# Optimization experiments

Measured on AMD Instinct MI355X. Metric: run time of the kernel, lower is better.

## Reference

```python
import jax, jax.numpy as jnp
import numpy as np

LN_EPS = 1e-5


def setup_inputs() -> dict:
    key = jax.random.key(0)
    ks = jax.random.split(key, 8)
    B, C, H, W = 16, 768, 64, 64
    cond_dim = 1024
    inp = {}
    inp["spatial_features"] = jax.random.normal(ks[0], (B, C, H, W), dtype=jnp.float32)
    inp["conditioning"] = jax.random.normal(ks[1], (B, cond_dim), dtype=jnp.float32)
    # conditioning_proj: Linear(cond_dim -> C)
    inp["w_cond"] = jax.random.normal(ks[2], (C, cond_dim), dtype=jnp.float32) * 0.02
    inp["b_cond"] = jnp.zeros((C,), dtype=jnp.float32)
    # MultiheadAttention packed in-projection [3C, C] and bias [3C]
    inp["in_proj_w"] = jax.random.normal(ks[3], (3 * C, C), dtype=jnp.float32) * 0.02
    inp["in_proj_b"] = jnp.zeros((3 * C,), dtype=jnp.float32)
    # MHA out_proj
    inp["attn_out_w"] = jax.random.normal(ks[4], (C, C), dtype=jnp.float32) * 0.02
    inp["attn_out_b"] = jnp.zeros((C,), dtype=jnp.float32)
    # output_proj Linear (dropout is identity at inference)
    inp["w_out"] = jax.random.normal(ks[5], (C, C), dtype=jnp.float32) * 0.02
    inp["b_out"] = jnp.zeros((C,), dtype=jnp.float32)
    # LayerNorm affine
    inp["ln_gamma"] = jnp.ones((C,), dtype=jnp.float32)
    inp["ln_beta"] = jnp.zeros((C,), dtype=jnp.float32)
    return inp


def reference(spatial_features, conditioning, w_cond, b_cond, in_proj_w, in_proj_b,
              attn_out_w, attn_out_b, w_out, b_out, ln_gamma, ln_beta):
    B, C, H, W = spatial_features.shape
    S = H * W
    # [B, C, H, W] -> [B, S, C]
    spatial_flat = spatial_features.reshape(B, C, S).transpose(0, 2, 1)
    # conditioning projection -> single KV token per batch: [B, C]
    cond = conditioning @ w_cond.T + b_cond
    # With a single key, softmax over the key axis is identically 1, so the
    # attention output is exactly the value vector broadcast over all queries;
    # Q and K projections have zero effect on output (and zero gradient).
    wv = in_proj_w[2 * C:]          # value rows of packed in-projection
    bv = in_proj_b[2 * C:]
    v = cond @ wv.T + bv            # [B, C]
    attn = v @ attn_out_w.T + attn_out_b  # MHA out_proj, [B, C]
    # output_proj (dropout = identity in eval)
    proj = attn @ w_out.T + b_out   # [B, C]
    # residual + LayerNorm over channel dim
    x = spatial_flat + proj[:, None, :]  # [B, S, C]
    mu = jnp.mean(x, axis=-1, keepdims=True)
    var = jnp.mean(jnp.square(x - mu), axis=-1, keepdims=True)
    y = (x - mu) * jax.lax.rsqrt(var + LN_EPS) * ln_gamma + ln_beta
    # [B, S, C] -> [B, C, H, W]
    return y.transpose(0, 2, 1).reshape(B, C, H, W)
```

## Files before the change

kernel.cpp:

```cpp
#include <hip/hip_runtime.h>

#define CDIM 768
#define SDIM 4096
#define SV (SDIM / 4)

typedef float nfloat4 __attribute__((ext_vector_type(4)));

__global__ __launch_bounds__(256) void small_gemm_kernel(
    const float* __restrict__ X, const float* __restrict__ W,
    const float* __restrict__ bias, float* __restrict__ out,
    int Cn, int K)
{
    int gid  = blockIdx.x * blockDim.x + threadIdx.x;
    int wid  = gid >> 6;
    int lane = threadIdx.x & 63;
    int total = 16 * Cn;
    if (wid >= total) return;
    int b = wid / Cn;
    int c = wid - b * Cn;
    const float* x = X + (size_t)b * K;
    const float* w = W + (size_t)c * K;
    float acc = 0.f;
    for (int k = lane * 4; k < K; k += 256) {
        float4 xv = *(const float4*)(x + k);
        float4 wv = *(const float4*)(w + k);
        acc += xv.x * wv.x + xv.y * wv.y + xv.z * wv.z + xv.w * wv.w;
    }
#pragma unroll
    for (int m = 32; m; m >>= 1) acc += __shfl_xor(acc, m, 64);
    if (lane == 0) out[wid] = acc + bias[c];
}

__global__ __launch_bounds__(512) void fused_add_ln_1pass(
    const float* __restrict__ sp, const float* __restrict__ proj,
    const float* __restrict__ gamma, const float* __restrict__ beta,
    float* __restrict__ out)
{
    __shared__ float s_proj[CDIM], s_gamma[CDIM], s_beta[CDIM];
    __shared__ float4 red_s[64][8];
    __shared__ float4 red_q[64][8];
    __shared__ float4 red2_s[8][8];
    __shared__ float4 red2_q[8][8];
    __shared__ float4 s_mu[8];
    __shared__ float4 s_rs[8];

    const int b  = blockIdx.y;
    const int s0 = blockIdx.x * 32;
    const int t  = threadIdx.x;
    for (int i = t; i < CDIM; i += 512) {
        s_proj[i]  = proj[b * CDIM + i];
        s_gamma[i] = gamma[i];
        s_beta[i]  = beta[i];
    }
    __syncthreads();

    const int si = t & 7;
    const int cg = t >> 3;
    const int c0 = cg * (CDIM / 64);

    const float4* spv  = (const float4*)(sp  + (size_t)b * CDIM * SDIM + s0) + (size_t)c0 * SV + si;
    nfloat4*      outv = (nfloat4*)     (out + (size_t)b * CDIM * SDIM + s0) + (size_t)c0 * SV + si;

    float4 x[12];
    float sx = 0, sy = 0, sz = 0, sw = 0;
    float qx = 0, qy = 0, qz = 0, qw = 0;
#pragma unroll
    for (int j = 0; j < 12; ++j) {
        float4 v = spv[(size_t)j * SV];
        float  p = s_proj[c0 + j];
        v.x += p; v.y += p; v.z += p; v.w += p;
        x[j] = v;
        sx += v.x; sy += v.y; sz += v.z; sw += v.w;
        qx += v.x * v.x; qy += v.y * v.y; qz += v.z * v.z; qw += v.w * v.w;
    }
    red_s[cg][si] = make_float4(sx, sy, sz, sw);
    red_q[cg][si] = make_float4(qx, qy, qz, qw);
    __syncthreads();

    if (t < 64) {
        const int si2 = t & 7;
        const int h   = t >> 3;
        float4 S = make_float4(0, 0, 0, 0), Q = make_float4(0, 0, 0, 0);
#pragma unroll
        for (int g = h * 8; g < h * 8 + 8; ++g) {
            float4 a = red_s[g][si2], q = red_q[g][si2];
            S.x += a.x; S.y += a.y; S.z += a.z; S.w += a.w;
            Q.x += q.x; Q.y += q.y; Q.z += q.z; Q.w += q.w;
        }
        red2_s[h][si2] = S;
        red2_q[h][si2] = Q;
    }
    __syncthreads();

    if (t < 8) {
        float4 S = make_float4(0, 0, 0, 0), Q = make_float4(0, 0, 0, 0);
#pragma unroll
        for (int h = 0; h < 8; ++h) {
            float4 a = red2_s[h][t], q = red2_q[h][t];
            S.x += a.x; S.y += a.y; S.z += a.z; S.w += a.w;
            Q.x += q.x; Q.y += q.y; Q.z += q.z; Q.w += q.w;
        }
        const float inv = 1.f / CDIM;
        float4 mu = make_float4(S.x * inv, S.y * inv, S.z * inv, S.w * inv);
        float4 rs;
        rs.x = rsqrtf(Q.x * inv - mu.x * mu.x + 1e-5f);
        rs.y = rsqrtf(Q.y * inv - mu.y * mu.y + 1e-5f);
        rs.z = rsqrtf(Q.z * inv - mu.z * mu.z + 1e-5f);
        rs.w = rsqrtf(Q.w * inv - mu.w * mu.w + 1e-5f);
        s_mu[t] = mu;
        s_rs[t] = rs;
    }
    __syncthreads();

    const float4 mu = s_mu[si];
    const float4 rs = s_rs[si];
#pragma unroll
    for (int j = 0; j < 12; ++j) {
        float g  = s_gamma[c0 + j];
        float be = s_beta[c0 + j];
        nfloat4 y;
        y.x = (x[j].x - mu.x) * rs.x * g + be;
        y.y = (x[j].y - mu.y) * rs.y * g + be;
        y.z = (x[j].z - mu.z) * rs.z * g + be;
        y.w = (x[j].w - mu.w) * rs.w * g + be;
        __builtin_nontemporal_store(y, &outv[(size_t)j * SV]);
    }
}

extern "C" void kernel_launch(void* const* d_in, const int* in_sizes, int n_in,
                              void* d_out, int out_size, void* d_ws, size_t ws_size,
                              hipStream_t stream) {
    const float* sp           = (const float*)d_in[0];
    const float* conditioning = (const float*)d_in[1];
    const float* w_cond       = (const float*)d_in[2];
    const float* b_cond       = (const float*)d_in[3];
    const float* in_proj_w    = (const float*)d_in[4];
    const float* in_proj_b    = (const float*)d_in[5];
    const float* attn_out_w   = (const float*)d_in[6];
    const float* attn_out_b   = (const float*)d_in[7];
    const float* w_out        = (const float*)d_in[8];
    const float* b_out        = (const float*)d_in[9];
    const float* ln_gamma     = (const float*)d_in[10];
    const float* ln_beta      = (const float*)d_in[11];
    float* out = (float*)d_out;
    float* ws  = (float*)d_ws;

    float* cond = ws;
    float* v    = ws + 12288;
    float* attn = ws + 24576;
    float* proj = ws + 36864;

    const int gemm_blocks = (16 * CDIM) / 4;
    small_gemm_kernel<<<gemm_blocks, 256, 0, stream>>>(
        conditioning, w_cond, b_cond, cond, CDIM, 1024);
    small_gemm_kernel<<<gemm_blocks, 256, 0, stream>>>(
        cond, in_proj_w + 2 * CDIM * CDIM, in_proj_b + 2 * CDIM, v, CDIM, CDIM);
    small_gemm_kernel<<<gemm_blocks, 256, 0, stream>>>(
        v, attn_out_w, attn_out_b, attn, CDIM, CDIM);
    small_gemm_kernel<<<gemm_blocks, 256, 0, stream>>>(
        attn, w_out, b_out, proj, CDIM, CDIM);

    dim3 grid(SDIM / 32, 16);
    fused_add_ln_1pass<<<grid, 512, 0, stream>>>(sp, proj, ln_gamma, ln_beta, out);
}
```

Measured before the change: 400.8 us.

## Fuse four chained small GEMV launches into one cooperative kernel with grid sync

Replaces four separate small GEMV kernel launches with a single cooperative kernel of 512 blocks. The blocks walk all output elements with a grid-stride loop and place a grid-wide barrier between stages. This removes three launch gaps and the tails between dependent kernels. The cost is grid.sync overhead, fewer waves in flight per stage (2048 waves covering 12288 outputs), and reliance on cooperative launch support.

```diff
diff --git a/kernel.cpp b/kernel.cpp
--- a/kernel.cpp
+++ b/kernel.cpp
@@ -1,4 +1,7 @@
 #include <hip/hip_runtime.h>
+#include <hip/hip_cooperative_groups.h>
+
+namespace cg = cooperative_groups;
 
 #define CDIM 768
 #define SDIM 4096
@@ -6,29 +9,52 @@
 
 typedef float nfloat4 __attribute__((ext_vector_type(4)));
 
-__global__ __launch_bounds__(256) void small_gemm_kernel(
+__device__ __forceinline__ void gemm16(
     const float* __restrict__ X, const float* __restrict__ W,
     const float* __restrict__ bias, float* __restrict__ out,
-    int Cn, int K)
+    int K, int wave, int nwaves, int lane)
 {
-    int gid  = blockIdx.x * blockDim.x + threadIdx.x;
-    int wid  = gid >> 6;
-    int lane = threadIdx.x & 63;
-    int total = 16 * Cn;
-    if (wid >= total) return;
-    int b = wid / Cn;
-    int c = wid - b * Cn;
-    const float* x = X + (size_t)b * K;
-    const float* w = W + (size_t)c * K;
-    float acc = 0.f;
-    for (int k = lane * 4; k < K; k += 256) {
-        float4 xv = *(const float4*)(x + k);
-        float4 wv = *(const float4*)(w + k);
-        acc += xv.x * wv.x + xv.y * wv.y + xv.z * wv.z + xv.w * wv.w;
+    for (int idx = wave; idx < 16 * CDIM; idx += nwaves) {
+        int b = idx / CDIM;
+        int c = idx - b * CDIM;
+        const float* x = X + (size_t)b * K;
+        const float* w = W + (size_t)c * K;
+        float acc = 0.f;
+        for (int k = lane * 4; k < K; k += 256) {
+            float4 xv = *(const float4*)(x + k);
+            float4 wv = *(const float4*)(w + k);
+            acc += xv.x * wv.x + xv.y * wv.y + xv.z * wv.z + xv.w * wv.w;
+        }
+#pragma unroll
+        for (int m = 32; m; m >>= 1) acc += __shfl_xor(acc, m, 64);
+        if (lane == 0) out[idx] = acc + bias[c];
     }
-#pragma unroll
-    for (int m = 32; m; m >>= 1) acc += __shfl_xor(acc, m, 64);
-    if (lane == 0) out[wid] = acc + bias[c];
+}
+
+__global__ __launch_bounds__(256) void gemm_chain_coop(
+    const float* __restrict__ conditioning,
+    const float* __restrict__ w_cond,  const float* __restrict__ b_cond,
+    const float* __restrict__ wv,      const float* __restrict__ bv,
+    const float* __restrict__ attn_w,  const float* __restrict__ attn_b,
+    const float* __restrict__ w_out,   const float* __restrict__ b_out,
+    float* __restrict__ cond, float* __restrict__ v,
+    float* __restrict__ attn, float* __restrict__ proj)
+{
+    cg::grid_group grid = cg::this_grid();
+    const int nwaves = (gridDim.x * blockDim.x) >> 6;
+    const int wave   = (blockIdx.x * blockDim.x + threadIdx.x) >> 6;
+    const int lane   = threadIdx.x & 63;
+
+    gemm16(conditioning, w_cond, b_cond, cond, 1024, wave, nwaves, lane);
+    __threadfence();
+    grid.sync();
+    gemm16(cond, wv, bv, v, CDIM, wave, nwaves, lane);
+    __threadfence();
+    grid.sync();
+    gemm16(v, attn_w, attn_b, attn, CDIM, wave, nwaves, lane);
+    __threadfence();
+    grid.sync();
+    gemm16(attn, w_out, b_out, proj, CDIM, wave, nwaves, lane);
 }
 
 __global__ __launch_bounds__(512) void fused_add_ln_1pass(
@@ -55,8 +81,8 @@
     __syncthreads();
 
     const int si = t & 7;
-    const int cg = t >> 3;
-    const int c0 = cg * (CDIM / 64);
+    const int cg2 = t >> 3;
+    const int c0 = cg2 * (CDIM / 64);
 
     const float4* spv  = (const float4*)(sp  + (size_t)b * CDIM * SDIM + s0) + (size_t)c0 * SV + si;
     nfloat4*      outv = (nfloat4*)     (out + (size_t)b * CDIM * SDIM + s0) + (size_t)c0 * SV + si;
@@ -73,8 +99,8 @@
         sx += v.x; sy += v.y; sz += v.z; sw += v.w;
         qx += v.x * v.x; qy += v.y * v.y; qz += v.z * v.z; qw += v.w * v.w;
     }
-    red_s[cg][si] = make_float4(sx, sy, sz, sw);
-    red_q[cg][si] = make_float4(qx, qy, qz, qw);
+    red_s[cg2][si] = make_float4(sx, sy, sz, sw);
+    red_q[cg2][si] = make_float4(qx, qy, qz, qw);
     __syncthreads();
 
     if (t < 64) {
@@ -150,15 +176,19 @@
     float* attn = ws + 24576;
     float* proj = ws + 36864;
 
-    const int gemm_blocks = (16 * CDIM) / 4;
-    small_gemm_kernel<<<gemm_blocks, 256, 0, stream>>>(
-        conditioning, w_cond, b_cond, cond, CDIM, 1024);
-    small_gemm_kernel<<<gemm_blocks, 256, 0, stream>>>(
-        cond, in_proj_w + 2 * CDIM * CDIM, in_proj_b + 2 * CDIM, v, CDIM, CDIM);
-    small_gemm_kernel<<<gemm_blocks, 256, 0, stream>>>(
-        v, attn_out_w, attn_out_b, attn, CDIM, CDIM);
-    small_gemm_kernel<<<gemm_blocks, 256, 0, stream>>>(
-        attn, w_out, b_out, proj, CDIM, CDIM);
+    const float* wv = in_proj_w + 2 * CDIM * CDIM;
+    const float* bv = in_proj_b + 2 * CDIM;
+
+    void* args[] = {
+        (void*)&conditioning,
+        (void*)&w_cond, (void*)&b_cond,
+        (void*)&wv,     (void*)&bv,
+        (void*)&attn_out_w, (void*)&attn_out_b,
+        (void*)&w_out,  (void*)&b_out,
+        (void*)&cond, (void*)&v, (void*)&attn, (void*)&proj,
+    };
+    hipLaunchCooperativeKernel((const void*)gemm_chain_coop,
+                               dim3(512), dim3(256), args, 0, stream);
 
     dim3 grid(SDIM / 32, 16);
     fused_add_ln_1pass<<<grid, 512, 0, stream>>>(sp, proj, ln_gamma, ln_beta, out);
```

Result: slower. 686.9 us (+71.4%).

## Use wave shuffles for LayerNorm reduction and shrink blocks to 256 threads

Applied to the files above, without the earlier changes.

Rewrites the per-token channel reduction in the add+LayerNorm kernel to use cross-lane xor shuffles within each wave, followed by a single small shared-memory combine across four waves. This drops two barrier stages and the serial reduction steps. Each block now covers 16 spatial positions with 256 threads instead of 32 with 512, so the grid is twice as large. Contiguous memory segments per channel row shrink to 64 bytes, which may reduce access efficiency.

```diff
diff --git a/kernel.cpp b/kernel.cpp
--- a/kernel.cpp
+++ b/kernel.cpp
@@ -31,89 +31,75 @@
     if (lane == 0) out[wid] = acc + bias[c];
 }
 
-__global__ __launch_bounds__(512) void fused_add_ln_1pass(
+__global__ __launch_bounds__(256) void fused_add_ln_v2(
     const float* __restrict__ sp, const float* __restrict__ proj,
     const float* __restrict__ gamma, const float* __restrict__ beta,
     float* __restrict__ out)
 {
     __shared__ float s_proj[CDIM], s_gamma[CDIM], s_beta[CDIM];
-    __shared__ float4 red_s[64][8];
-    __shared__ float4 red_q[64][8];
-    __shared__ float4 red2_s[8][8];
-    __shared__ float4 red2_q[8][8];
-    __shared__ float4 s_mu[8];
-    __shared__ float4 s_rs[8];
+    __shared__ float4 red_s[4][4];
+    __shared__ float4 red_q[4][4];
 
     const int b  = blockIdx.y;
-    const int s0 = blockIdx.x * 32;
+    const int s0 = blockIdx.x * 16;
     const int t  = threadIdx.x;
-    for (int i = t; i < CDIM; i += 512) {
+    for (int i = t; i < CDIM; i += 256) {
         s_proj[i]  = proj[b * CDIM + i];
         s_gamma[i] = gamma[i];
         s_beta[i]  = beta[i];
     }
     __syncthreads();
 
-    const int si = t & 7;
-    const int cg = t >> 3;
+    const int si = t & 3;
+    const int cg = t >> 2;
     const int c0 = cg * (CDIM / 64);
 
     const float4* spv  = (const float4*)(sp  + (size_t)b * CDIM * SDIM + s0) + (size_t)c0 * SV + si;
     nfloat4*      outv = (nfloat4*)     (out + (size_t)b * CDIM * SDIM + s0) + (size_t)c0 * SV + si;
 
     float4 x[12];
-    float sx = 0, sy = 0, sz = 0, sw = 0;
-    float qx = 0, qy = 0, qz = 0, qw = 0;
+    float4 S = make_float4(0, 0, 0, 0);
+    float4 Q = make_float4(0, 0, 0, 0);
 #pragma unroll
     for (int j = 0; j < 12; ++j) {
         float4 v = spv[(size_t)j * SV];
         float  p = s_proj[c0 + j];
         v.x += p; v.y += p; v.z += p; v.w += p;
         x[j] = v;
-        sx += v.x; sy += v.y; sz += v.z; sw += v.w;
-        qx += v.x * v.x; qy += v.y * v.y; qz += v.z * v.z; qw += v.w * v.w;
+        S.x += v.x; S.y += v.y; S.z += v.z; S.w += v.w;
+        Q.x += v.x * v.x; Q.y += v.y * v.y; Q.z += v.z * v.z; Q.w += v.w * v.w;
     }
-    red_s[cg][si] = make_float4(sx, sy, sz, sw);
-    red_q[cg][si] = make_float4(qx, qy, qz, qw);
-    __syncthreads();
 
-    if (t < 64) {
-        const int si2 = t & 7;
-        const int h   = t >> 3;
-        float4 S = make_float4(0, 0, 0, 0), Q = make_float4(0, 0, 0, 0);
 #pragma unroll
-        for (int g = h * 8; g < h * 8 + 8; ++g) {
-            float4 a = red_s[g][si2], q = red_q[g][si2];
-            S.x += a.x; S.y += a.y; S.z += a.z; S.w += a.w;
-            Q.x += q.x; Q.y += q.y; Q.z += q.z; Q.w += q.w;
-        }
-        red2_s[h][si2] = S;
-        red2_q[h][si2] = Q;
+    for (int m = 4; m <= 32; m <<= 1) {
+        S.x += __shfl_xor(S.x, m, 64); S.y += __shfl_xor(S.y, m, 64);
+        S.z += __shfl_xor(S.z, m, 64); S.w += __shfl_xor(S.w, m, 64);
+        Q.x += __shfl_xor(Q.x, m, 64); Q.y += __shfl_xor(Q.y, m, 64);
+        Q.z += __shfl_xor(Q.z, m, 64); Q.w += __shfl_xor(Q.w, m, 64);
+    }
+    const int wave = t >> 6;
+    const int lane = t & 63;
+    if (lane < 4) {
+        red_s[wave][lane] = S;
+        red_q[wave][lane] = Q;
     }
     __syncthreads();
 
-    if (t < 8) {
-        float4 S = make_float4(0, 0, 0, 0), Q = make_float4(0, 0, 0, 0);
+    float4 Sa = make_float4(0, 0, 0, 0), Qa = make_float4(0, 0, 0, 0);
 #pragma unroll
-        for (int h = 0; h < 8; ++h) {
-            float4 a = red2_s[h][t], q = red2_q[h][t];
-            S.x += a.x; S.y += a.y; S.z += a.z; S.w += a.w;
-            Q.x += q.x; Q.y += q.y; Q.z += q.z; Q.w += q.w;
-        }
-        const float inv = 1.f / CDIM;
-        float4 mu = make_float4(S.x * inv, S.y * inv, S.z * inv, S.w * inv);
-        float4 rs;
-        rs.x = rsqrtf(Q.x * inv - mu.x * mu.x + 1e-5f);
-        rs.y = rsqrtf(Q.y * inv - mu.y * mu.y + 1e-5f);
-        rs.z = rsqrtf(Q.z * inv - mu.z * mu.z + 1e-5f);
-        rs.w = rsqrtf(Q.w * inv - mu.w * mu.w + 1e-5f);
-        s_mu[t] = mu;
-        s_rs[t] = rs;
+    for (int g = 0; g < 4; ++g) {
+        float4 a = red_s[g][si], q = red_q[g][si];
+        Sa.x += a.x; Sa.y += a.y; Sa.z += a.z; Sa.w += a.w;
+        Qa.x += q.x; Qa.y += q.y; Qa.z += q.z; Qa.w += q.w;
     }
-    __syncthreads();
+    const float inv = 1.f / CDIM;
+    float4 mu = make_float4(Sa.x * inv, Sa.y * inv, Sa.z * inv, Sa.w * inv);
+    float4 rs;
+    rs.x = rsqrtf(Qa.x * inv - mu.x * mu.x + 1e-5f);
+    rs.y = rsqrtf(Qa.y * inv - mu.y * mu.y + 1e-5f);
+    rs.z = rsqrtf(Qa.z * inv - mu.z * mu.z + 1e-5f);
+    rs.w = rsqrtf(Qa.w * inv - mu.w * mu.w + 1e-5f);
 
-    const float4 mu = s_mu[si];
-    const float4 rs = s_rs[si];
 #pragma unroll
     for (int j = 0; j < 12; ++j) {
         float g  = s_gamma[c0 + j];
@@ -160,6 +146,6 @@
     small_gemm_kernel<<<gemm_blocks, 256, 0, stream>>>(
         attn, w_out, b_out, proj, CDIM, CDIM);
 
-    dim3 grid(SDIM / 32, 16);
-    fused_add_ln_1pass<<<grid, 512, 0, stream>>>(sp, proj, ln_gamma, ln_beta, out);
+    dim3 grid(SDIM / 16, 16);
+    fused_add_ln_v2<<<grid, 256, 0, stream>>>(sp, proj, ln_gamma, ln_beta, out);
 }
```

Measured after the change: 424.9 us. +6.0%, slower.
